# Performance work log

Hardware: AMD Instinct MI355X
Metric: run time of the kernel (lower is better)

The kernel has to match this reference:

```python
import jax, jax.numpy as jnp
import numpy as np

N_GROUPS = 4


def setup_inputs() -> dict:
    key = jax.random.key(0)
    ks = jax.random.split(key, 6)
    I, J, B = 512, 512, 4  # query tokens, key tokens, grid batch (B = 1 * n_groups)
    n_dim, out_per_group = 128, 4  # n_heads // n_groups = 16 // 4
    grid_q = jax.random.normal(ks[0], (I, 3), dtype=jnp.float32)
    grid_kv = jax.random.normal(ks[1], (B, J, 3), dtype=jnp.float32)
    W1 = jax.random.normal(ks[2], (3, n_dim), dtype=jnp.float32) * (1.0 / np.sqrt(3))
    b1 = jnp.zeros((n_dim,), dtype=jnp.float32)
    W2 = jax.random.normal(ks[3], (n_dim, n_dim), dtype=jnp.float32) * (1.0 / np.sqrt(n_dim))
    b2 = jnp.zeros((n_dim,), dtype=jnp.float32)
    W3 = jax.random.normal(ks[4], (n_dim, out_per_group), dtype=jnp.float32) * (1.0 / np.sqrt(n_dim))
    b3 = jnp.zeros((out_per_group,), dtype=jnp.float32)
    return {"grid_q": grid_q, "grid_kv": grid_kv, "W1": W1, "b1": b1,
            "W2": W2, "b2": b2, "W3": W3, "b3": b3}


def reference(grid_q, grid_kv, W1, b1, W2, b2, W3, b3):
    # grid_q: [I, 3] -> [1, I, 3]; grid_kv: [B, J, 3]
    gq = grid_q[None, :, :]
    # pairwise position difference: [B, I, J, 3]
    pos = gq[:, :, None, :] - grid_kv[:, None, :, :]
    # sign-log transform
    bias = jnp.sign(pos) * jnp.log1p(jnp.abs(pos))
    # tiny MLP: 3 -> n_dim -> n_dim -> heads//groups, pointwise over (B, I, J)
    h = jax.nn.relu(jnp.einsum('bijc,cd->bijd', bias, W1) + b1)
    h = jax.nn.relu(jnp.einsum('bijd,de->bije', h, W2) + b2)
    out = jnp.einsum('bije,eo->bijo', h, W3) + b3  # [B, I, J, O]
    # rearrange '(b g) i j o -> b (g o) i j' with g = N_GROUPS
    B, I, J, O = out.shape
    out = out.reshape(B // N_GROUPS, N_GROUPS, I, J, O)
    out = jnp.transpose(out, (0, 1, 4, 2, 3)).reshape(B // N_GROUPS, N_GROUPS * O, I, J)
    return out
```

## Files before the change

kernel.cpp:

```cpp
#include <hip/hip_runtime.h>
#include <math.h>

#define NDIM 128
#define TILE 64
#define NBLOCKS 2048
#define POS_PER_BLOCK 512
#define ITERS 8
#define CH 512

typedef __attribute__((ext_vector_type(8)))  short  short8;
typedef __attribute__((ext_vector_type(4)))  float  float4v;
typedef __attribute__((ext_vector_type(16))) float  float16;

__device__ __forceinline__ unsigned cvt_pk(float lo, float hi) {
    unsigned r;
    asm("v_cvt_pk_bf16_f32 %0, %1, %2" : "=v"(r) : "v"(lo), "v"(hi));
    return r;
}

__device__ __forceinline__ int kmap(int c, int jj) {
    return 32 * (c >> 2) + 16 * ((c >> 1) & 1) + 4 * (c & 1) + ((jj >> 2) << 3) + (jj & 3);
}

__global__ __launch_bounds__(256, 3)
void crpb_mfma3(const float* __restrict__ gq,
                const float* __restrict__ gkv,
                const float* __restrict__ W1,
                const float* __restrict__ b1,
                const float* __restrict__ W2,
                const float* __restrict__ b2,
                const float* __restrict__ W3,
                const float* __restrict__ b3,
                float* __restrict__ out)
{
    __shared__ __align__(16) unsigned short ash[16 * CH];
    __shared__ __align__(16) unsigned short h2s[16 * CH];
    __shared__ __align__(16) float b2s[NDIM];

    const int tid   = threadIdx.x;
    const int lane  = tid & 63;
    const int w     = __builtin_amdgcn_readfirstlane(tid >> 6);
    const int l31   = lane & 31;
    const int lhalf = lane >> 5;
    const int m16   = lane & 15;
    const int q16   = lane >> 4;

    if (tid < NDIM) b2s[tid] = b2[tid];

    const int pt  = w & 1;
    const int ct0 = (w >> 1) * 2;

    short8 a2f0[8], a2f1[8];
    #pragma unroll
    for (int ks = 0; ks < 8; ++ks) {
        const int c = 2 * ks + lhalf;
        unsigned t0[4], t1[4];
        #pragma unroll
        for (int t = 0; t < 4; ++t) {
            const int d0 = kmap(c, 2 * t), d1 = d0 + 1;
            const int e0 = ct0 * 32 + l31, e1 = e0 + 32;
            t0[t] = cvt_pk(W2[d0 * 128 + e0], W2[d1 * 128 + e0]);
            t1[t] = cvt_pk(W2[d0 * 128 + e1], W2[d1 * 128 + e1]);
        }
        __builtin_memcpy(&a2f0[ks], t0, 16);
        __builtin_memcpy(&a2f1[ks], t1, 16);
    }

    short8 w3t[4];
    #pragma unroll
    for (int ks = 0; ks < 4; ++ks) {
        const int c = ks * 4 + q16;
        unsigned tt[4];
        #pragma unroll
        for (int t = 0; t < 4; ++t) {
            const int k0 = kmap(c, 2 * t), k1 = k0 + 1;
            const float lo = (m16 < 4) ? W3[k0 * 4 + m16] : 0.0f;
            const float hi = (m16 < 4) ? W3[k1 * 4 + m16] : 0.0f;
            tt[t] = cvt_pk(lo, hi);
        }
        __builtin_memcpy(&w3t[ks], tt, 16);
    }
    float b3v[4];
    #pragma unroll
    for (int r = 0; r < 4; ++r) b3v[r] = (q16 == 0) ? b3[r] : 0.0f;

    __syncthreads();

    const int posblock = blockIdx.x * POS_PER_BLOCK;
    const int bb = posblock >> 18;
    const int i  = (posblock >> 9) & 511;
    const float q0 = gq[i * 3 + 0], q1 = gq[i * 3 + 1], q2 = gq[i * 3 + 2];

    unsigned short* aw        = ash + 4 * w * CH + lane * 8;
    const unsigned short* br  = ash + lhalf * CH + (pt * 32 + l31) * 8;
    unsigned short* cw        = h2s + (ct0 * 4 + lhalf) * CH + (pt * 32 + l31) * 8;
    const unsigned short* dr  = h2s + q16 * CH + (w * 16 + m16) * 8;

    const float* kvp0 = gkv + (size_t)((bb << 9) + lane) * 3;
    float* obase = out + (((size_t)bb) << 20) + ((size_t)i << 9) + w * 16 + m16;

    for (int it = 0; it < ITERS; ++it) {
        const int jb = it * TILE;

        {
            const float* kvp = kvp0 + jb * 3;
            const float d0 = q0 - kvp[0], d1 = q1 - kvp[1], d2 = q2 - kvp[2];
            const float f0 = copysignf(__logf(1.0f + fabsf(d0)), d0);
            const float f1 = copysignf(__logf(1.0f + fabsf(d1)), d1);
            const float f2 = copysignf(__logf(1.0f + fabsf(d2)), d2);
            #pragma unroll
            for (int u = 0; u < 4; ++u) {
                const int c = 4 * w + u;
                unsigned pk[4];
                #pragma unroll
                for (int t = 0; t < 4; ++t) {
                    const int ch0 = kmap(c, 2 * t), ch1 = ch0 + 1;
                    float h0 = fmaf(f2, W1[256 + ch0], fmaf(f1, W1[128 + ch0],
                               fmaf(f0, W1[ch0], b1[ch0])));
                    float h1 = fmaf(f2, W1[256 + ch1], fmaf(f1, W1[128 + ch1],
                               fmaf(f0, W1[ch1], b1[ch1])));
                    pk[t] = cvt_pk(fmaxf(h0, 0.0f), fmaxf(h1, 0.0f));
                }
                short8 v; __builtin_memcpy(&v, pk, 16);
                *(short8*)(aw + u * CH) = v;
            }
        }
        __syncthreads();

        float16 acc0, acc1;
        #pragma unroll
        for (int qr = 0; qr < 4; ++qr) {
            float4v i0 = *(const float4v*)&b2s[ct0 * 32 + 8 * qr + 4 * lhalf];
            float4v i1 = *(const float4v*)&b2s[ct0 * 32 + 32 + 8 * qr + 4 * lhalf];
            #pragma unroll
            for (int t = 0; t < 4; ++t) { acc0[4 * qr + t] = i0[t]; acc1[4 * qr + t] = i1[t]; }
        }
        #pragma unroll
        for (int ks = 0; ks < 8; ++ks) {
            short8 bfrag = *(const short8*)(br + ks * 2 * CH);
            acc0 = __builtin_amdgcn_mfma_f32_32x32x16_bf16(a2f0[ks], bfrag, acc0, 0, 0, 0);
            acc1 = __builtin_amdgcn_mfma_f32_32x32x16_bf16(a2f1[ks], bfrag, acc1, 0, 0, 0);
        }

        {
            unsigned p0[4], p1[4], p2[4], p3[4];
            #pragma unroll
            for (int t = 0; t < 4; ++t) {
                p0[t] = cvt_pk(fmaxf(acc0[2 * t], 0.f),     fmaxf(acc0[2 * t + 1], 0.f));
                p1[t] = cvt_pk(fmaxf(acc0[8 + 2 * t], 0.f), fmaxf(acc0[8 + 2 * t + 1], 0.f));
                p2[t] = cvt_pk(fmaxf(acc1[2 * t], 0.f),     fmaxf(acc1[2 * t + 1], 0.f));
                p3[t] = cvt_pk(fmaxf(acc1[8 + 2 * t], 0.f), fmaxf(acc1[8 + 2 * t + 1], 0.f));
            }
            short8 v0, v1, v2, v3;
            __builtin_memcpy(&v0, p0, 16); __builtin_memcpy(&v1, p1, 16);
            __builtin_memcpy(&v2, p2, 16); __builtin_memcpy(&v3, p3, 16);
            *(short8*)(cw + 0 * CH) = v0;
            *(short8*)(cw + 2 * CH) = v1;
            *(short8*)(cw + 4 * CH) = v2;
            *(short8*)(cw + 6 * CH) = v3;
        }
        __syncthreads();

        {
            float4v acc3;
            #pragma unroll
            for (int r = 0; r < 4; ++r) acc3[r] = b3v[r];
            #pragma unroll
            for (int ks = 0; ks < 4; ++ks) {
                short8 bfrag = *(const short8*)(dr + ks * 4 * CH);
                acc3 = __builtin_amdgcn_mfma_f32_16x16x32_bf16(w3t[ks], bfrag, acc3, 0, 0, 0);
            }
            if (q16 == 0) {
                #pragma unroll
                for (int r = 0; r < 4; ++r)
                    obase[(size_t)(r << 18) + jb] = acc3[r];
            }
        }
    }
}

extern "C" void kernel_launch(void* const* d_in, const int* in_sizes, int n_in,
                              void* d_out, int out_size, void* d_ws, size_t ws_size,
                              hipStream_t stream) {
    const float* gq  = (const float*)d_in[0];
    const float* gkv = (const float*)d_in[1];
    const float* W1  = (const float*)d_in[2];
    const float* b1  = (const float*)d_in[3];
    const float* W2  = (const float*)d_in[4];
    const float* b2  = (const float*)d_in[5];
    const float* W3  = (const float*)d_in[6];
    const float* b3  = (const float*)d_in[7];
    float* out = (float*)d_out;

    crpb_mfma3<<<NBLOCKS, 256, 0, stream>>>(gq, gkv, W1, b1, W2, b2, W3, b3, out);
}
```

Before: 133.1 us.

## Reassign layer-2 MFMA work so each wave owns one output column tile

```diff
diff --git a/kernel.cpp b/kernel.cpp
--- a/kernel.cpp
+++ b/kernel.cpp
@@ -23,7 +23,7 @@
 }
 
 __global__ __launch_bounds__(256, 3)
-void crpb_mfma3(const float* __restrict__ gq,
+void crpb_mfma4(const float* __restrict__ gq,
                 const float* __restrict__ gkv,
                 const float* __restrict__ W1,
                 const float* __restrict__ b1,
@@ -47,23 +47,20 @@
 
     if (tid < NDIM) b2s[tid] = b2[tid];
 
-    const int pt  = w & 1;
-    const int ct0 = (w >> 1) * 2;
+    const int ct = w;
 
-    short8 a2f0[8], a2f1[8];
+    short8 a2f[8];
     #pragma unroll
     for (int ks = 0; ks < 8; ++ks) {
         const int c = 2 * ks + lhalf;
-        unsigned t0[4], t1[4];
+        unsigned t0[4];
         #pragma unroll
         for (int t = 0; t < 4; ++t) {
             const int d0 = kmap(c, 2 * t), d1 = d0 + 1;
-            const int e0 = ct0 * 32 + l31, e1 = e0 + 32;
+            const int e0 = ct * 32 + l31;
             t0[t] = cvt_pk(W2[d0 * 128 + e0], W2[d1 * 128 + e0]);
-            t1[t] = cvt_pk(W2[d0 * 128 + e1], W2[d1 * 128 + e1]);
         }
-        __builtin_memcpy(&a2f0[ks], t0, 16);
-        __builtin_memcpy(&a2f1[ks], t1, 16);
+        __builtin_memcpy(&a2f[ks], t0, 16);
     }
 
     short8 w3t[4];
@@ -92,19 +89,23 @@
     const float q0 = gq[i * 3 + 0], q1 = gq[i * 3 + 1], q2 = gq[i * 3 + 2];
 
     unsigned short* aw        = ash + 4 * w * CH + lane * 8;
-    const unsigned short* br  = ash + lhalf * CH + (pt * 32 + l31) * 8;
-    unsigned short* cw        = h2s + (ct0 * 4 + lhalf) * CH + (pt * 32 + l31) * 8;
+    const unsigned short* br  = ash + lhalf * CH + l31 * 8;
+    unsigned short* cw        = h2s + (4 * ct + lhalf) * CH + l31 * 8;
     const unsigned short* dr  = h2s + q16 * CH + (w * 16 + m16) * 8;
 
     const float* kvp0 = gkv + (size_t)((bb << 9) + lane) * 3;
     float* obase = out + (((size_t)bb) << 20) + ((size_t)i << 9) + w * 16 + m16;
 
+    float kv0 = kvp0[0], kv1 = kvp0[1], kv2 = kvp0[2];
+
     for (int it = 0; it < ITERS; ++it) {
         const int jb = it * TILE;
 
         {
-            const float* kvp = kvp0 + jb * 3;
-            const float d0 = q0 - kvp[0], d1 = q1 - kvp[1], d2 = q2 - kvp[2];
+            const float d0 = q0 - kv0, d1 = q1 - kv1, d2 = q2 - kv2;
+            const float* kvn = kvp0 + ((it + 1) & 7) * (TILE * 3);
+            kv0 = kvn[0]; kv1 = kvn[1]; kv2 = kvn[2];
+
             const float f0 = copysignf(__logf(1.0f + fabsf(d0)), d0);
             const float f1 = copysignf(__logf(1.0f + fabsf(d1)), d1);
             const float f2 = copysignf(__logf(1.0f + fabsf(d2)), d2);
@@ -130,16 +131,16 @@
         float16 acc0, acc1;
         #pragma unroll
         for (int qr = 0; qr < 4; ++qr) {
-            float4v i0 = *(const float4v*)&b2s[ct0 * 32 + 8 * qr + 4 * lhalf];
-            float4v i1 = *(const float4v*)&b2s[ct0 * 32 + 32 + 8 * qr + 4 * lhalf];
+            float4v i0 = *(const float4v*)&b2s[ct * 32 + 8 * qr + 4 * lhalf];
             #pragma unroll
-            for (int t = 0; t < 4; ++t) { acc0[4 * qr + t] = i0[t]; acc1[4 * qr + t] = i1[t]; }
+            for (int t = 0; t < 4; ++t) { acc0[4 * qr + t] = i0[t]; acc1[4 * qr + t] = i0[t]; }
         }
         #pragma unroll
         for (int ks = 0; ks < 8; ++ks) {
-            short8 bfrag = *(const short8*)(br + ks * 2 * CH);
-            acc0 = __builtin_amdgcn_mfma_f32_32x32x16_bf16(a2f0[ks], bfrag, acc0, 0, 0, 0);
-            acc1 = __builtin_amdgcn_mfma_f32_32x32x16_bf16(a2f1[ks], bfrag, acc1, 0, 0, 0);
+            short8 bf0 = *(const short8*)(br + ks * 2 * CH);
+            short8 bf1 = *(const short8*)(br + ks * 2 * CH + 256);
+            acc0 = __builtin_amdgcn_mfma_f32_32x32x16_bf16(a2f[ks], bf0, acc0, 0, 0, 0);
+            acc1 = __builtin_amdgcn_mfma_f32_32x32x16_bf16(a2f[ks], bf1, acc1, 0, 0, 0);
         }
 
         {
@@ -156,8 +157,8 @@
             __builtin_memcpy(&v2, p2, 16); __builtin_memcpy(&v3, p3, 16);
             *(short8*)(cw + 0 * CH) = v0;
             *(short8*)(cw + 2 * CH) = v1;
-            *(short8*)(cw + 4 * CH) = v2;
-            *(short8*)(cw + 6 * CH) = v3;
+            *(short8*)(cw + 0 * CH + 256) = v2;
+            *(short8*)(cw + 2 * CH + 256) = v3;
         }
         __syncthreads();
 
@@ -192,5 +193,5 @@
     const float* b3  = (const float*)d_in[7];
     float* out = (float*)d_out;
 
-    crpb_mfma3<<<NBLOCKS, 256, 0, stream>>>(gq, gkv, W1, b1, W2, b2, W3, b3, out);
+    crpb_mfma4<<<NBLOCKS, 256, 0, stream>>>(gq, gkv, W1, b1, W2, b2, W3, b3, out);
 }
```

New measurement: 127.2 us. -4.4%, faster.
